# Kernel tuning notes

Measured on AMD Instinct MI355X. Metric: run time of the kernel, lower is better.

The kernel has to match this reference:

```python
import jax, jax.numpy as jnp
import numpy as np

B, S = 64, 256
VOCAB, DL, DA, DV = 30522, 300, 74, 35
DH, GH, LH, RH = 128, 64, 128, 128  # modality dim, proj-GRU hidden, LSTM hidden, RGN hidden


def _gru_dir(x, Wi, Wh, bi, bh):
    # x: [B,S,D] -> [B,S,H]; torch GRU gate order (r, z, n)
    xg = x @ Wi + bi  # [B,S,3H] precomputed input projections
    H = Wh.shape[0]
    def step(h, xg_t):
        hg = h @ Wh + bh
        xr, xz, xn = jnp.split(xg_t, 3, axis=-1)
        hr, hz, hn = jnp.split(hg, 3, axis=-1)
        r = jax.nn.sigmoid(xr + hr)
        z = jax.nn.sigmoid(xz + hz)
        n = jnp.tanh(xn + r * hn)
        h = (1.0 - z) * n + z * h
        return h, h
    h0 = jnp.zeros((x.shape[0], H), x.dtype)
    _, ys = jax.lax.scan(step, h0, jnp.swapaxes(xg, 0, 1))
    return jnp.swapaxes(ys, 0, 1)


def _bigru(x, Wi, Wh, bi, bh):
    f = _gru_dir(x, Wi[0], Wh[0], bi[0], bh[0])
    b = _gru_dir(x[:, ::-1], Wi[1], Wh[1], bi[1], bh[1])[:, ::-1]
    return jnp.concatenate([f, b], axis=-1)


def _lstm_dir(x, Wi, Wh, bi, bh):
    xg = x @ Wi + bi  # [B,S,4H]; torch LSTM gate order (i, f, g, o)
    H = Wh.shape[0]
    def step(carry, xg_t):
        h, c = carry
        g = xg_t + h @ Wh + bh
        i, f, gg, o = jnp.split(g, 4, axis=-1)
        c = jax.nn.sigmoid(f) * c + jax.nn.sigmoid(i) * jnp.tanh(gg)
        h = jax.nn.sigmoid(o) * jnp.tanh(c)
        return (h, c), h
    z = jnp.zeros((x.shape[0], H), x.dtype)
    _, ys = jax.lax.scan(step, (z, z), jnp.swapaxes(xg, 0, 1))
    return jnp.swapaxes(ys, 0, 1)


def _bilstm(x, Wi, Wh, bi, bh):
    f = _lstm_dir(x, Wi[0], Wh[0], bi[0], bh[0])
    b = _lstm_dir(x[:, ::-1], Wi[1], Wh[1], bi[1], bh[1])[:, ::-1]
    return jnp.concatenate([f, b], axis=-1)


def _rgn_scan(x, h0, Wx, Wh, b):
    # RGNCell: gated recurrent cell (GRU-style), returns final state [B,H]
    xg = x @ Wx + b  # [B,S,3H]
    def step(h, xg_t):
        hg = h @ Wh
        xr, xz, xn = jnp.split(xg_t, 3, axis=-1)
        hr, hz, hn = jnp.split(hg, 3, axis=-1)
        r = jax.nn.sigmoid(xr + hr)
        z = jax.nn.sigmoid(xz + hz)
        n = jnp.tanh(xn + r * hn)
        return (1.0 - z) * n + z * h, None
    h, _ = jax.lax.scan(step, h0, jnp.swapaxes(xg, 0, 1))
    return h


def _xattn(q, kv):
    # parameter-free scaled dot-product cross-modal attention (JCAF)
    scale = 1.0 / np.sqrt(q.shape[-1]).astype(np.float32)
    s = jnp.einsum('bsd,btd->bst', q, kv) * scale
    return jnp.einsum('bst,btd->bsd', jax.nn.softmax(s, axis=-1), kv)


def _forward(sentences, acoustic, video, state0, state1, emb,
             proj_l_W, proj_l_b, proj_a_W, proj_a_b, proj_v_W, proj_v_b,
             gru_Wi, gru_Wh, gru_bi, gru_bh,
             lstm_Wi, lstm_Wh, lstm_bi, lstm_bh,
             rgn_Wx, rgn_Wh, rgn_b, fc1_W, fc1_b, fc2_W, fc2_b):
    enc = emb[sentences]                          # LanguageEmbeddingLayer: [B,S,DL]
    # SeqEncoder: project each modality to 128-d (dropout off in eval)
    seq_l = enc @ proj_l_W + proj_l_b             # [B,S,128]
    seq_a = acoustic @ proj_a_W + proj_a_b
    seq_v = video @ proj_v_W + proj_v_b
    # project_l/a/v: bidirectional GRU 128 -> 2*64 = 128
    x_l = _bigru(seq_l, gru_Wi[0], gru_Wh[0], gru_bi[0], gru_bh[0])
    x_a = _bigru(seq_a, gru_Wi[1], gru_Wh[1], gru_bi[1], gru_bh[1])
    x_v = _bigru(seq_v, gru_Wi[2], gru_Wh[2], gru_bi[2], gru_bh[2])
    # JCAF: each modality enriched by cross-attention to the other two
    fin_txt = x_l + _xattn(x_l, x_a) + _xattn(x_l, x_v)
    fin_aud = x_a + _xattn(x_a, x_l) + _xattn(x_a, x_v)
    fin_vis = x_v + _xattn(x_v, x_l) + _xattn(x_v, x_a)
    tstep = jnp.concatenate([fin_txt, fin_aud, fin_vis], axis=-1)      # [B,S,384]
    step_fusion = _bilstm(tstep, lstm_Wi, lstm_Wh, lstm_bi, lstm_bh)   # [B,S,256]
    # two custom RGNCell recurrences: forward sweep + reversed sweep
    out0 = _rgn_scan(step_fusion, state0, rgn_Wx[0], rgn_Wh[0], rgn_b[0])
    out1 = _rgn_scan(step_fusion[:, ::-1], state1, rgn_Wx[1], rgn_Wh[1], rgn_b[1])
    h = jax.nn.leaky_relu((out0 + out1) @ fc1_W + fc1_b)
    return h @ fc2_W + fc2_b                     # [B,1]


def setup_inputs():
    keys = iter(jax.random.split(jax.random.key(0), 48))
    def rn(shape, s=0.05):
        return jax.random.normal(next(keys), shape, jnp.float32) * s
    return {
        'sentences': jax.random.randint(next(keys), (B, S), 0, VOCAB),
        'acoustic': jax.random.normal(next(keys), (B, S, DA), jnp.float32),
        'video': jax.random.normal(next(keys), (B, S, DV), jnp.float32),
        'state0': jax.random.normal(next(keys), (B, RH), jnp.float32),
        'state1': jax.random.normal(next(keys), (B, RH), jnp.float32),
        'emb': rn((VOCAB, DL), 0.1),
        'proj_l_W': rn((DL, DH)), 'proj_l_b': rn((DH,)),
        'proj_a_W': rn((DA, DH)), 'proj_a_b': rn((DH,)),
        'proj_v_W': rn((DV, DH)), 'proj_v_b': rn((DH,)),
        'gru_Wi': rn((3, 2, DH, 3 * GH)), 'gru_Wh': rn((3, 2, GH, 3 * GH)),
        'gru_bi': rn((3, 2, 3 * GH)), 'gru_bh': rn((3, 2, 3 * GH)),
        'lstm_Wi': rn((2, 3 * DH, 4 * LH)), 'lstm_Wh': rn((2, LH, 4 * LH)),
        'lstm_bi': rn((2, 4 * LH)), 'lstm_bh': rn((2, 4 * LH)),
        'rgn_Wx': rn((2, 2 * LH, 3 * RH)), 'rgn_Wh': rn((2, RH, 3 * RH)),
        'rgn_b': rn((2, 3 * RH)),
        'fc1_W': rn((RH, 32)), 'fc1_b': rn((32,)),
        'fc2_W': rn((32, 1)), 'fc2_b': rn((1,)),
    }


def reference(sentences, acoustic, video, state0, state1, emb,
              proj_l_W, proj_l_b, proj_a_W, proj_a_b, proj_v_W, proj_v_b,
              gru_Wi, gru_Wh, gru_bi, gru_bh,
              lstm_Wi, lstm_Wh, lstm_bi, lstm_bh,
              rgn_Wx, rgn_Wh, rgn_b, fc1_W, fc1_b, fc2_W, fc2_b):
    return _forward(sentences, acoustic, video, state0, state1, emb,
                    proj_l_W, proj_l_b, proj_a_W, proj_a_b, proj_v_W, proj_v_b,
                    gru_Wi, gru_Wh, gru_bi, gru_bh,
                    lstm_Wi, lstm_Wh, lstm_bi, lstm_bh,
                    rgn_Wx, rgn_Wh, rgn_b, fc1_W, fc1_b, fc2_W, fc2_b)
```

## Files before the change

kernel.cpp:

```cpp
#include <hip/hip_runtime.h>

#define WS_SEQ      0LL
#define WS_XGGRU    6291456LL
#define WS_X        0LL
#define WS_TSTEP    18874368LL
#define WS_S        6291456LL
#define WS_XGLSTM   0LL
#define WS_SF       16777216LL
#define WS_XGRGN    0LL
#define WS_OUT0     20971520LL

__device__ __forceinline__ float sigf(float x) {
    return __builtin_amdgcn_rcpf(1.f + __expf(-x));
}
__device__ __forceinline__ float tanhfast(float x) {
    float e = __expf(2.f * x);
    return 1.f - 2.f * __builtin_amdgcn_rcpf(e + 1.f);
}
__device__ __forceinline__ float rl(float v, int i) {
    return __int_as_float(__builtin_amdgcn_readlane(__float_as_int(v), i));
}

typedef float vf16 __attribute__((ext_vector_type(16)));
typedef float vf2 __attribute__((ext_vector_type(2)));

#define LD16(V, P, S) { _Pragma("unroll") \
    for (int _j = 0; _j < 16; ++_j) (V)[_j] = (P)[_j * (S)]; }
#define DOT16(ACC, V, H, B) { _Pragma("unroll") \
    for (int _j = 0; _j < 16; ++_j) (ACC) = fmaf(rl((H), (B) + _j), (V)[_j], (ACC)); }

__device__ __forceinline__ void gemm_body(
    const float* __restrict__ Ab, int lda, const int* __restrict__ idx,
    const float* __restrict__ Wb, int wld, int wtrans,
    const float* __restrict__ bb,
    float* __restrict__ Cb, int ldc,
    int K, float alpha, int accum)
{
    int m0 = blockIdx.y * 64, n0 = blockIdx.x * 64;
    int t = threadIdx.x;
    int tx = t & 7, ty = t >> 3;

    __shared__ __align__(16) float As[16][68];
    __shared__ __align__(16) float Ws[16][68];

    vf2 acc2[8][4];
#pragma unroll
    for (int i = 0; i < 8; ++i)
#pragma unroll
        for (int j = 0; j < 4; ++j) acc2[i][j] = (vf2){0.f, 0.f};

    long long arow[4];
#pragma unroll
    for (int i = 0; i < 4; ++i) {
        int m = (t + i * 64) >> 2;
        arow[i] = idx ? (long long)idx[m0 + m] : (long long)(m0 + m);
    }
    const bool a_vec = ((lda & 3) == 0);

    auto loadA = [&](int k0, float4* r) {
#pragma unroll
        for (int i = 0; i < 4; ++i) {
            int j = t + i * 64;
            int kq = j & 3;
            int kk = k0 + kq * 4;
            const float* p = Ab + arow[i] * (long long)lda + kk;
            float4 v = {0.f, 0.f, 0.f, 0.f};
            if (a_vec && kk + 3 < K) {
                v = *(const float4*)p;
            } else {
                if (kk + 0 < K) v.x = p[0];
                if (kk + 1 < K) v.y = p[1];
                if (kk + 2 < K) v.z = p[2];
                if (kk + 3 < K) v.w = p[3];
            }
            r[i] = v;
        }
    };
    auto loadW = [&](int k0, float4* r) {
        if (!wtrans) {
#pragma unroll
            for (int i = 0; i < 4; ++i) {
                int j = t + i * 64;
                int k = j >> 4, nq = j & 15;
                float4 v = {0.f, 0.f, 0.f, 0.f};
                if (k0 + k < K)
                    v = *(const float4*)(Wb + (long long)(k0 + k) * wld + n0 + nq * 4);
                r[i] = v;
            }
        } else {
#pragma unroll
            for (int i = 0; i < 4; ++i) {
                int j = t + i * 64;
                int n = j >> 2, kq = j & 3;
                int kk = k0 + kq * 4;
                const float* p = Wb + (long long)(n0 + n) * wld + kk;
                float4 v = {0.f, 0.f, 0.f, 0.f};
                if (kk + 3 < K) v = *(const float4*)p;
                else {
                    if (kk + 0 < K) v.x = p[0];
                    if (kk + 1 < K) v.y = p[1];
                    if (kk + 2 < K) v.z = p[2];
                    if (kk + 3 < K) v.w = p[3];
                }
                r[i] = v;
            }
        }
    };

    float4 aR[4], wR[4];
    loadA(0, aR);
    loadW(0, wR);

    for (int k0 = 0; k0 < K; k0 += 16) {
#pragma unroll
        for (int i = 0; i < 4; ++i) {
            int j = t + i * 64;
            int m = j >> 2, kq = j & 3;
            As[kq * 4 + 0][m] = aR[i].x; As[kq * 4 + 1][m] = aR[i].y;
            As[kq * 4 + 2][m] = aR[i].z; As[kq * 4 + 3][m] = aR[i].w;
        }
        if (!wtrans) {
#pragma unroll
            for (int i = 0; i < 4; ++i) {
                int j = t + i * 64;
                int k = j >> 4, nq = j & 15;
                *(float4*)&Ws[k][nq * 4] = wR[i];
            }
        } else {
#pragma unroll
            for (int i = 0; i < 4; ++i) {
                int j = t + i * 64;
                int n = j >> 2, kq = j & 3;
                Ws[kq * 4 + 0][n] = wR[i].x; Ws[kq * 4 + 1][n] = wR[i].y;
                Ws[kq * 4 + 2][n] = wR[i].z; Ws[kq * 4 + 3][n] = wR[i].w;
            }
        }
        __syncthreads();
        if (k0 + 16 < K) {
            loadA(k0 + 16, aR);
            loadW(k0 + 16, wR);
        }
#pragma unroll
        for (int k = 0; k < 16; ++k) {
            float4 a0 = *(const float4*)&As[k][ty * 8];
            float4 a1 = *(const float4*)&As[k][ty * 8 + 4];
            float4 b0 = *(const float4*)&Ws[k][tx * 8];
            float4 b1 = *(const float4*)&Ws[k][tx * 8 + 4];
            float av[8] = {a0.x, a0.y, a0.z, a0.w, a1.x, a1.y, a1.z, a1.w};
            vf2 bv[4];
            bv[0] = (vf2){b0.x, b0.y}; bv[1] = (vf2){b0.z, b0.w};
            bv[2] = (vf2){b1.x, b1.y}; bv[3] = (vf2){b1.z, b1.w};
#pragma unroll
            for (int i = 0; i < 8; ++i) {
                vf2 a2 = {av[i], av[i]};
#pragma unroll
                for (int j = 0; j < 4; ++j)
                    acc2[i][j] = __builtin_elementwise_fma(a2, bv[j], acc2[i][j]);
            }
        }
        __syncthreads();
    }

#pragma unroll
    for (int i = 0; i < 8; ++i) {
        long long gm = m0 + ty * 8 + i;
#pragma unroll
        for (int jq = 0; jq < 2; ++jq) {
            float* cp = Cb + gm * ldc + n0 + tx * 8 + jq * 4;
            float4 v;
            v.x = alpha * acc2[i][jq * 2 + 0][0];
            v.y = alpha * acc2[i][jq * 2 + 0][1];
            v.z = alpha * acc2[i][jq * 2 + 1][0];
            v.w = alpha * acc2[i][jq * 2 + 1][1];
            if (bb) {
                const float* bp = bb + n0 + tx * 8 + jq * 4;
                v.x += bp[0]; v.y += bp[1]; v.z += bp[2]; v.w += bp[3];
            }
            if (accum) {
                float4 o = *(const float4*)cp;
                v.x += o.x; v.y += o.y; v.z += o.z; v.w += o.w;
            }
            *(float4*)cp = v;
        }
    }
}

__global__ __launch_bounds__(64) void gemm_k(
    const float* __restrict__ A, long long a_z, int a_zdiv, int lda,
    const int* __restrict__ idx,
    const float* __restrict__ W, long long w_z, int wld, int wtrans,
    const float* __restrict__ bias, int bias_z,
    float* __restrict__ C, long long c_z, int ldc,
    int K, float alpha, int accum)
{
    int z = blockIdx.z;
    gemm_body(A + (long long)(z / a_zdiv) * a_z, lda, idx,
              W + (long long)z * w_z, wld, wtrans,
              bias ? bias + (long long)z * bias_z : nullptr,
              C + (long long)z * c_z, ldc, K, alpha, accum);
}

__global__ __launch_bounds__(64) void att_score_k(
    const float* __restrict__ X, float* __restrict__ S,
    int q0, int q1, int q2, int k0, int k1, int k2)
{
    int z = blockIdx.z;
    int pair = z >> 6, b = z & 63;
    int qi = pair == 0 ? q0 : (pair == 1 ? q1 : q2);
    int ki = pair == 0 ? k0 : (pair == 1 ? k1 : k2);
    gemm_body(X + (long long)qi * 2097152 + (long long)b * 32768, 128, nullptr,
              X + (long long)ki * 2097152 + (long long)b * 32768, 128, 1,
              nullptr,
              S + (long long)z * 65536, 256, 128, 0.08838834764831845f, 0);
}

__global__ __launch_bounds__(64) void att_apply_k(
    const float* __restrict__ S, const float* __restrict__ X,
    float* __restrict__ tstep,
    int q0, int q1, int q2, int k0, int k1, int k2)
{
    int z = blockIdx.z;
    int pair = z >> 6, b = z & 63;
    int qi = pair == 0 ? q0 : (pair == 1 ? q1 : q2);
    int ki = pair == 0 ? k0 : (pair == 1 ? k1 : k2);
    gemm_body(S + (long long)z * 65536, 256, nullptr,
              X + (long long)ki * 2097152 + (long long)b * 32768, 128, 0,
              nullptr,
              tstep + (long long)qi * 128 + (long long)b * 98304, 384,
              256, 1.f, 1);
}

__global__ __launch_bounds__(256) void copy_tstep_k(const float* __restrict__ x,
                                                    float* __restrict__ tstep)
{
    int o = blockIdx.x * 256 + threadIdx.x;
    int c = o % 384;
    int row = o / 384;
    int m = c >> 7, cc = c & 127;
    tstep[o] = x[(long long)m * 2097152 + (long long)row * 128 + cc];
}

__global__ __launch_bounds__(256) void softmax_k(float* __restrict__ S)
{
    int wave = threadIdx.x >> 6, lane = threadIdx.x & 63;
    int row = blockIdx.x * 4 + wave;
    float* p = S + (long long)row * 256;
    float v[4];
    float mx = -1e30f;
#pragma unroll
    for (int i = 0; i < 4; ++i) { v[i] = p[lane + i * 64]; mx = fmaxf(mx, v[i]); }
#pragma unroll
    for (int off = 32; off > 0; off >>= 1) mx = fmaxf(mx, __shfl_xor(mx, off));
    float sum = 0.f;
#pragma unroll
    for (int i = 0; i < 4; ++i) { v[i] = __expf(v[i] - mx); sum += v[i]; }
#pragma unroll
    for (int off = 32; off > 0; off >>= 1) sum += __shfl_xor(sum, off);
    float inv = 1.f / sum;
#pragma unroll
    for (int i = 0; i < 4; ++i) p[lane + i * 64] = v[i] * inv;
}

__global__ __launch_bounds__(192) void gru_rec_k(const float* __restrict__ xg,
                                                 const float* __restrict__ Wh,
                                                 const float* __restrict__ bh,
                                                 float* __restrict__ xout)
{
    int b = blockIdx.x, z = blockIdx.y;
    int m = z >> 1, d = z & 1;
    int tid = threadIdx.x, lane = tid & 63;
    int c = tid;
    const float* Whz = Wh + (long long)z * 12288;
    const float* wp = Whz + c;
    vf16 W0, W1, W2, W3;
    LD16(W0, wp + 0 * 16 * 192, 192); LD16(W1, wp + 1 * 16 * 192, 192);
    LD16(W2, wp + 2 * 16 * 192, 192); LD16(W3, wp + 3 * 16 * 192, 192);
    float bias = bh[z * 192 + c];

    __shared__ float g[2][192];
    int n = lane;
    float h = 0.f;
    const float* xgb = xg + (long long)z * 3145728 + (long long)b * 49152;
    float* xob = xout + (long long)m * 2097152 + (long long)b * 32768 + d * 64;
    int tt0 = d ? 255 : 0;
    const float* xr0 = xgb + tt0 * 192;
    float x_r = xr0[n], x_z = xr0[64 + n], x_n = xr0[128 + n];

#pragma unroll 1
    for (int t = 0; t < 256; ++t) {
        int tt = d ? 255 - t : t;
        float nx_r = 0, nx_z = 0, nx_n = 0;
        if (t < 255) {
            const float* xr = xgb + (d ? tt - 1 : tt + 1) * 192;
            nx_r = xr[n]; nx_z = xr[64 + n]; nx_n = xr[128 + n];
        }
        float s0 = bias, s1 = 0.f, s2 = 0.f, s3 = 0.f;
        DOT16(s0, W0, h, 0);  DOT16(s1, W1, h, 16);
        DOT16(s2, W2, h, 32); DOT16(s3, W3, h, 48);
        g[t & 1][c] = (s0 + s1) + (s2 + s3);
        __syncthreads();
        const float* gp = g[t & 1];
        float r  = sigf(x_r + gp[n]);
        float zz = sigf(x_z + gp[64 + n]);
        float nn = tanhfast(x_n + r * gp[128 + n]);
        h = (1.f - zz) * nn + zz * h;
        if (c < 64) xob[tt * 128 + n] = h;
        x_r = nx_r; x_z = nx_z; x_n = nx_n;
    }
}

__global__ __launch_bounds__(512) void lstm_rec_k(const float* __restrict__ xg,
                                                  const float* __restrict__ Wh,
                                                  const float* __restrict__ bh,
                                                  float* __restrict__ sf)
{
    int b = blockIdx.x, d = blockIdx.y;
    int tid = threadIdx.x, lane = tid & 63;
    int kh = tid >> 8;
    int cp = tid & 255;
    const float* Whz = Wh + (long long)d * 65536;

    __shared__ __align__(16) float wlds[36864];
    __shared__ float part[2][1024];
    for (int i = tid; i < 9216; i += 512) {
        int row = i >> 7, c4 = (i & 127) << 2;
        int srow = row < 36 ? row : row + 28;
        *(float4*)&wlds[row * 512 + c4] = *(const float4*)(Whz + srow * 512 + c4);
    }
    const float* wl  = wlds + (kh * 36) * 512 + 2 * cp;
    const float* wpg = Whz + (long long)(kh * 64 + 36) * 512 + 2 * cp;

    int n = kh * 64 + lane;
    float h = 0.f, cst = 0.f;
    const float* xgb = xg + (long long)d * 8388608 + (long long)b * 131072;
    float* sfb = sf + (long long)b * 65536 + d * 128;

    vf2 bias2 = {0.f, 0.f}, xc2 = {0.f, 0.f};
    if (kh == 0) {
        bias2 = *(const vf2*)(bh + d * 512 + 2 * cp);
        int tt0 = d ? 255 : 0;
        xc2 = *(const vf2*)(xgb + tt0 * 512 + 2 * cp);
    }
    __syncthreads();

#pragma unroll 1
    for (int t = 0; t < 256; ++t) {
        int tt = d ? 255 - t : t;
        vf2 nxc2 = {0.f, 0.f};
        if (kh == 0 && t < 255)
            nxc2 = *(const vf2*)(xgb + (d ? tt - 1 : tt + 1) * 512 + 2 * cp);
        vf2 a0 = xc2 + bias2, a1 = {0.f, 0.f};
#pragma unroll
        for (int r = 0; r < 36; ++r) {
            float hs = rl(h, r);
            vf2 hb = {hs, hs};
            vf2 w = *(const vf2*)(wl + r * 512);
            if (r & 1) a1 = __builtin_elementwise_fma(hb, w, a1);
            else       a0 = __builtin_elementwise_fma(hb, w, a0);
        }
#pragma unroll
        for (int r = 0; r < 28; ++r) {
            float hs = rl(h, 36 + r);
            vf2 hb = {hs, hs};
            vf2 w = *(const vf2*)(wpg + r * 512);
            if (r & 1) a1 = __builtin_elementwise_fma(hb, w, a1);
            else       a0 = __builtin_elementwise_fma(hb, w, a0);
        }
        *(vf2*)&part[t & 1][kh * 512 + 2 * cp] = a0 + a1;
        __syncthreads();
        const float* p = part[t & 1];
        float iv = p[n]       + p[512 + n];
        float fv = p[128 + n] + p[512 + 128 + n];
        float gv = p[256 + n] + p[512 + 256 + n];
        float ov = p[384 + n] + p[512 + 384 + n];
        cst = sigf(fv) * cst + sigf(iv) * tanhfast(gv);
        h = sigf(ov) * tanhfast(cst);
        if (cp < 64) sfb[tt * 256 + n] = h;
        xc2 = nxc2;
    }
}

__global__ __launch_bounds__(768) void rgn_rec_k(const float* __restrict__ xg,
                                                 const float* __restrict__ Wh,
                                                 const float* __restrict__ state0,
                                                 const float* __restrict__ state1,
                                                 float* __restrict__ outbase)
{
    int b = blockIdx.x, d = blockIdx.y;
    int tid = threadIdx.x, lane = tid & 63;
    int kh = (tid >= 384) ? 1 : 0;
    int c  = tid - kh * 384;
    const float* Whz = Wh + (long long)d * 49152;
    const float* wp = Whz + (long long)(kh * 64) * 384 + c;
    vf16 W0, W1, W2, W3;
    LD16(W0, wp + 0 * 16 * 384, 384); LD16(W1, wp + 1 * 16 * 384, 384);
    LD16(W2, wp + 2 * 16 * 384, 384); LD16(W3, wp + 3 * 16 * 384, 384);

    __shared__ float part[2][768];
    int n = kh * 64 + lane;
    const float* st = d ? state1 : state0;
    float h = st[b * 128 + n];
    const float* xgb = xg + (long long)d * 6291456 + (long long)b * 98304;
    int tt0 = d ? 255 : 0;
    const float* xr0 = xgb + tt0 * 384;
    float x_r = xr0[n], x_z = xr0[128 + n], x_n = xr0[256 + n];

#pragma unroll 1
    for (int t = 0; t < 256; ++t) {
        int tt = d ? 255 - t : t;
        float nx_r = 0, nx_z = 0, nx_n = 0;
        if (t < 255) {
            const float* xr = xgb + (d ? tt - 1 : tt + 1) * 384;
            nx_r = xr[n]; nx_z = xr[128 + n]; nx_n = xr[256 + n];
        }
        float s0 = 0.f, s1 = 0.f, s2 = 0.f, s3 = 0.f;
        DOT16(s0, W0, h, 0);  DOT16(s1, W1, h, 16);
        DOT16(s2, W2, h, 32); DOT16(s3, W3, h, 48);
        part[t & 1][kh * 384 + c] = (s0 + s1) + (s2 + s3);
        __syncthreads();
        const float* p = part[t & 1];
        float pr = p[n]       + p[384 + n];
        float pz = p[128 + n] + p[384 + 128 + n];
        float pn = p[256 + n] + p[384 + 256 + n];
        float r  = sigf(x_r + pr);
        float zz = sigf(x_z + pz);
        float nn = tanhfast(x_n + r * pn);
        h = (1.f - zz) * nn + zz * h;
        x_r = nx_r; x_z = nx_z; x_n = nx_n;
    }
    if (c < 64) outbase[(long long)d * 8192 + b * 128 + n] = h;
}

__global__ __launch_bounds__(256) void fc_k(const float* __restrict__ o01,
                                            const float* __restrict__ f1W,
                                            const float* __restrict__ f1b,
                                            const float* __restrict__ f2W,
                                            const float* __restrict__ f2b,
                                            float* __restrict__ out)
{
    __shared__ float s[8192];
    __shared__ float h1[2048];
    int tid = threadIdx.x;
    for (int e = tid; e < 8192; e += 256) s[e] = o01[e] + o01[8192 + e];
    __syncthreads();
    for (int o = tid; o < 2048; o += 256) {
        int b = o >> 5, q = o & 31;
        float acc = f1b[q];
        for (int k = 0; k < 128; ++k) acc += s[b * 128 + k] * f1W[k * 32 + q];
        h1[o] = acc >= 0.f ? acc : 0.01f * acc;
    }
    __syncthreads();
    if (tid < 64) {
        float acc = f2b[0];
        for (int q = 0; q < 32; ++q) acc += h1[tid * 32 + q] * f2W[q];
        out[tid] = acc;
    }
}

extern "C" void kernel_launch(void* const* d_in, const int* in_sizes, int n_in,
                              void* d_out, int out_size, void* d_ws, size_t ws_size,
                              hipStream_t stream)
{
    const int*   sent     = (const int*)  d_in[0];
    const float* acoustic = (const float*)d_in[1];
    const float* video    = (const float*)d_in[2];
    const float* state0   = (const float*)d_in[3];
    const float* state1   = (const float*)d_in[4];
    const float* emb      = (const float*)d_in[5];
    const float* plW = (const float*)d_in[6],  *plb = (const float*)d_in[7];
    const float* paW = (const float*)d_in[8],  *pab = (const float*)d_in[9];
    const float* pvW = (const float*)d_in[10], *pvb = (const float*)d_in[11];
    const float* gWi = (const float*)d_in[12], *gWh = (const float*)d_in[13];
    const float* gbi = (const float*)d_in[14], *gbh = (const float*)d_in[15];
    const float* lWi = (const float*)d_in[16], *lWh = (const float*)d_in[17];
    const float* lbi = (const float*)d_in[18], *lbh = (const float*)d_in[19];
    const float* rWx = (const float*)d_in[20], *rWh = (const float*)d_in[21];
    const float* rb  = (const float*)d_in[22];
    const float* f1W = (const float*)d_in[23], *f1b = (const float*)d_in[24];
    const float* f2W = (const float*)d_in[25], *f2b = (const float*)d_in[26];
    float* ws  = (float*)d_ws;
    float* out = (float*)d_out;

    dim3 blk(64);

    gemm_k<<<dim3(2, 256, 1), blk, 0, stream>>>(emb, 0, 1, 300, sent,
        plW, 0, 128, 0, plb, 0, ws + WS_SEQ, 0, 128, 300, 1.f, 0);
    gemm_k<<<dim3(2, 256, 1), blk, 0, stream>>>(acoustic, 0, 1, 74, nullptr,
        paW, 0, 128, 0, pab, 0, ws + WS_SEQ + 2097152, 0, 128, 74, 1.f, 0);
    gemm_k<<<dim3(2, 256, 1), blk, 0, stream>>>(video, 0, 1, 35, nullptr,
        pvW, 0, 128, 0, pvb, 0, ws + WS_SEQ + 4194304, 0, 128, 35, 1.f, 0);

    gemm_k<<<dim3(3, 256, 6), blk, 0, stream>>>(ws + WS_SEQ, 2097152, 2, 128, nullptr,
        gWi, 24576, 192, 0, gbi, 192, ws + WS_XGGRU, 3145728, 192, 128, 1.f, 0);

    gru_rec_k<<<dim3(64, 6), dim3(192), 0, stream>>>(ws + WS_XGGRU, gWh, gbh, ws + WS_X);

    copy_tstep_k<<<dim3(24576), dim3(256), 0, stream>>>(ws + WS_X, ws + WS_TSTEP);

    att_score_k<<<dim3(4, 4, 192), blk, 0, stream>>>(ws + WS_X, ws + WS_S,
        0, 1, 2, 1, 0, 0);
    softmax_k<<<dim3(12288), dim3(256), 0, stream>>>(ws + WS_S);
    att_apply_k<<<dim3(2, 4, 192), blk, 0, stream>>>(ws + WS_S, ws + WS_X,
        ws + WS_TSTEP, 0, 1, 2, 1, 0, 0);
    att_score_k<<<dim3(4, 4, 192), blk, 0, stream>>>(ws + WS_X, ws + WS_S,
        0, 1, 2, 2, 2, 1);
    softmax_k<<<dim3(12288), dim3(256), 0, stream>>>(ws + WS_S);
    att_apply_k<<<dim3(2, 4, 192), blk, 0, stream>>>(ws + WS_S, ws + WS_X,
        ws + WS_TSTEP, 0, 1, 2, 2, 2, 1);

    gemm_k<<<dim3(8, 256, 2), blk, 0, stream>>>(ws + WS_TSTEP, 0, 1, 384, nullptr,
        lWi, 196608, 512, 0, lbi, 512, ws + WS_XGLSTM, 8388608, 512, 384, 1.f, 0);

    lstm_rec_k<<<dim3(64, 2), dim3(512), 0, stream>>>(ws + WS_XGLSTM, lWh, lbh, ws + WS_SF);

    gemm_k<<<dim3(6, 256, 2), blk, 0, stream>>>(ws + WS_SF, 0, 1, 256, nullptr,
        rWx, 98304, 384, 0, rb, 384, ws + WS_XGRGN, 6291456, 384, 256, 1.f, 0);

    rgn_rec_k<<<dim3(64, 2), dim3(768), 0, stream>>>(ws + WS_XGRGN, rWh, state0, state1,
                                                     ws + WS_OUT0);

    fc_k<<<dim3(1), dim3(256), 0, stream>>>(ws + WS_OUT0, f1W, f1b, f2W, f2b, out);
}
```

Before: 1.451 ms.

## Double-buffer GEMM shared tiles, merge projection launches, fuse tstep copy into attention

The shared GEMM body now ping-pongs two LDS tile buffers, so the next tile is written after compute and only one barrier is needed per k-step. The three modality projection GEMMs are merged into a single launch indexed by blockIdx.z. The separate copy kernel that seeded the tstep buffer is removed; the first attention-apply pass instead adds the query features in its epilogue and writes rather than accumulates. This cuts launches and a full extra pass over memory, at the cost of doubled LDS per block, which may lower occupancy.

```diff
diff --git a/kernel.cpp b/kernel.cpp
--- a/kernel.cpp
+++ b/kernel.cpp
@@ -33,6 +33,7 @@
     const float* __restrict__ Ab, int lda, const int* __restrict__ idx,
     const float* __restrict__ Wb, int wld, int wtrans,
     const float* __restrict__ bb,
+    const float* __restrict__ initsrc, int ldi,
     float* __restrict__ Cb, int ldc,
     int K, float alpha, int accum)
 {
@@ -40,8 +41,8 @@
     int t = threadIdx.x;
     int tx = t & 7, ty = t >> 3;
 
-    __shared__ __align__(16) float As[16][68];
-    __shared__ __align__(16) float Ws[16][68];
+    __shared__ __align__(16) float As[2][16][68];
+    __shared__ __align__(16) float Ws[2][16][68];
 
     vf2 acc2[8][4];
 #pragma unroll
@@ -106,46 +107,52 @@
             }
         }
     };
+    auto writeT = [&](int buf, const float4* aR, const float4* wR) {
+#pragma unroll
+        for (int i = 0; i < 4; ++i) {
+            int j = t + i * 64;
+            int m = j >> 2, kq = j & 3;
+            As[buf][kq * 4 + 0][m] = aR[i].x; As[buf][kq * 4 + 1][m] = aR[i].y;
+            As[buf][kq * 4 + 2][m] = aR[i].z; As[buf][kq * 4 + 3][m] = aR[i].w;
+        }
+        if (!wtrans) {
+#pragma unroll
+            for (int i = 0; i < 4; ++i) {
+                int j = t + i * 64;
+                int k = j >> 4, nq = j & 15;
+                *(float4*)&Ws[buf][k][nq * 4] = wR[i];
+            }
+        } else {
+#pragma unroll
+            for (int i = 0; i < 4; ++i) {
+                int j = t + i * 64;
+                int n = j >> 2, kq = j & 3;
+                Ws[buf][kq * 4 + 0][n] = wR[i].x; Ws[buf][kq * 4 + 1][n] = wR[i].y;
+                Ws[buf][kq * 4 + 2][n] = wR[i].z; Ws[buf][kq * 4 + 3][n] = wR[i].w;
+            }
+        }
+    };
 
     float4 aR[4], wR[4];
     loadA(0, aR);
     loadW(0, wR);
-
-    for (int k0 = 0; k0 < K; k0 += 16) {
-#pragma unroll
-        for (int i = 0; i < 4; ++i) {
-            int j = t + i * 64;
-            int m = j >> 2, kq = j & 3;
-            As[kq * 4 + 0][m] = aR[i].x; As[kq * 4 + 1][m] = aR[i].y;
-            As[kq * 4 + 2][m] = aR[i].z; As[kq * 4 + 3][m] = aR[i].w;
-        }
-        if (!wtrans) {
-#pragma unroll
-            for (int i = 0; i < 4; ++i) {
-                int j = t + i * 64;
-                int k = j >> 4, nq = j & 15;
-                *(float4*)&Ws[k][nq * 4] = wR[i];
-            }
-        } else {
-#pragma unroll
-            for (int i = 0; i < 4; ++i) {
-                int j = t + i * 64;
-                int n = j >> 2, kq = j & 3;
-                Ws[kq * 4 + 0][n] = wR[i].x; Ws[kq * 4 + 1][n] = wR[i].y;
-                Ws[kq * 4 + 2][n] = wR[i].z; Ws[kq * 4 + 3][n] = wR[i].w;
-            }
-        }
-        __syncthreads();
-        if (k0 + 16 < K) {
-            loadA(k0 + 16, aR);
-            loadW(k0 + 16, wR);
+    writeT(0, aR, wR);
+    __syncthreads();
+
+    int nt = (K + 15) >> 4;
+    for (int ti = 0; ti < nt; ++ti) {
+        int cur = ti & 1;
+        bool more = (ti + 1 < nt);
+        if (more) {
+            loadA((ti + 1) * 16, aR);
+            loadW((ti + 1) * 16, wR);
         }
 #pragma unroll
         for (int k = 0; k < 16; ++k) {
-            float4 a0 = *(const float4*)&As[k][ty * 8];
-            float4 a1 = *(const float4*)&As[k][ty * 8 + 4];
-            float4 b0 = *(const float4*)&Ws[k][tx * 8];
-            float4 b1 = *(const float4*)&Ws[k][tx * 8 + 4];
+            float4 a0 = *(const float4*)&As[cur][k][ty * 8];
+            float4 a1 = *(const float4*)&As[cur][k][ty * 8 + 4];
+            float4 b0 = *(const float4*)&Ws[cur][k][tx * 8];
+            float4 b1 = *(const float4*)&Ws[cur][k][tx * 8 + 4];
             float av[8] = {a0.x, a0.y, a0.z, a0.w, a1.x, a1.y, a1.z, a1.w};
             vf2 bv[4];
             bv[0] = (vf2){b0.x, b0.y}; bv[1] = (vf2){b0.z, b0.w};
@@ -158,7 +165,10 @@
                     acc2[i][j] = __builtin_elementwise_fma(a2, bv[j], acc2[i][j]);
             }
         }
-        __syncthreads();
+        if (more) {
+            writeT(cur ^ 1, aR, wR);
+            __syncthreads();
+        }
     }
 
 #pragma unroll
@@ -166,15 +176,20 @@
         long long gm = m0 + ty * 8 + i;
 #pragma unroll
         for (int jq = 0; jq < 2; ++jq) {
-            float* cp = Cb + gm * ldc + n0 + tx * 8 + jq * 4;
+            int col = n0 + tx * 8 + jq * 4;
+            float* cp = Cb + gm * ldc + col;
             float4 v;
             v.x = alpha * acc2[i][jq * 2 + 0][0];
             v.y = alpha * acc2[i][jq * 2 + 0][1];
             v.z = alpha * acc2[i][jq * 2 + 1][0];
             v.w = alpha * acc2[i][jq * 2 + 1][1];
             if (bb) {
-                const float* bp = bb + n0 + tx * 8 + jq * 4;
+                const float* bp = bb + col;
                 v.x += bp[0]; v.y += bp[1]; v.z += bp[2]; v.w += bp[3];
+            }
+            if (initsrc) {
+                const float* ip = initsrc + gm * (long long)ldi + col;
+                v.x += ip[0]; v.y += ip[1]; v.z += ip[2]; v.w += ip[3];
             }
             if (accum) {
                 float4 o = *(const float4*)cp;
@@ -196,8 +211,28 @@
     int z = blockIdx.z;
     gemm_body(A + (long long)(z / a_zdiv) * a_z, lda, idx,
               W + (long long)z * w_z, wld, wtrans,
-              bias ? bias + (long long)z * bias_z : nullptr,
+              bias ? bias + (long long)z * bias_z : nullptr, nullptr, 0,
               C + (long long)z * c_z, ldc, K, alpha, accum);
+}
+
+__global__ __launch_bounds__(64) void proj3_k(
+    const int* __restrict__ sent, const float* __restrict__ emb,
+    const float* __restrict__ acoustic, const float* __restrict__ video,
+    const float* __restrict__ plW, const float* __restrict__ plb,
+    const float* __restrict__ paW, const float* __restrict__ pab,
+    const float* __restrict__ pvW, const float* __restrict__ pvb,
+    float* __restrict__ seq)
+{
+    int z = blockIdx.z;
+    const float* A; int lda; const int* ix; const float* W; const float* bi;
+    float* C; int K;
+    if (z == 0) { A = emb;      lda = 300; ix = sent;    W = plW; bi = plb;
+                  C = seq;               K = 300; }
+    else if (z == 1) { A = acoustic; lda = 74;  ix = nullptr; W = paW; bi = pab;
+                  C = seq + 2097152;     K = 74; }
+    else        { A = video;    lda = 35;  ix = nullptr; W = pvW; bi = pvb;
+                  C = seq + 4194304;     K = 35; }
+    gemm_body(A, lda, ix, W, 128, 0, bi, nullptr, 0, C, 128, K, 1.f, 0);
 }
 
 __global__ __launch_bounds__(64) void att_score_k(
@@ -210,34 +245,26 @@
     int ki = pair == 0 ? k0 : (pair == 1 ? k1 : k2);
     gemm_body(X + (long long)qi * 2097152 + (long long)b * 32768, 128, nullptr,
               X + (long long)ki * 2097152 + (long long)b * 32768, 128, 1,
-              nullptr,
+              nullptr, nullptr, 0,
               S + (long long)z * 65536, 256, 128, 0.08838834764831845f, 0);
 }
 
 __global__ __launch_bounds__(64) void att_apply_k(
     const float* __restrict__ S, const float* __restrict__ X,
     float* __restrict__ tstep,
-    int q0, int q1, int q2, int k0, int k1, int k2)
+    int q0, int q1, int q2, int k0, int k1, int k2, int doinit)
 {
     int z = blockIdx.z;
     int pair = z >> 6, b = z & 63;
     int qi = pair == 0 ? q0 : (pair == 1 ? q1 : q2);
     int ki = pair == 0 ? k0 : (pair == 1 ? k1 : k2);
+    const float* initsrc = doinit
+        ? X + (long long)qi * 2097152 + (long long)b * 32768 : nullptr;
     gemm_body(S + (long long)z * 65536, 256, nullptr,
               X + (long long)ki * 2097152 + (long long)b * 32768, 128, 0,
-              nullptr,
+              nullptr, initsrc, 128,
               tstep + (long long)qi * 128 + (long long)b * 98304, 384,
-              256, 1.f, 1);
-}
-
-__global__ __launch_bounds__(256) void copy_tstep_k(const float* __restrict__ x,
-                                                    float* __restrict__ tstep)
-{
-    int o = blockIdx.x * 256 + threadIdx.x;
-    int c = o % 384;
-    int row = o / 384;
-    int m = c >> 7, cc = c & 127;
-    tstep[o] = x[(long long)m * 2097152 + (long long)row * 128 + cc];
+              256, 1.f, doinit ? 0 : 1);
 }
 
 __global__ __launch_bounds__(256) void softmax_k(float* __restrict__ S)
@@ -483,30 +510,24 @@
 
     dim3 blk(64);
 
-    gemm_k<<<dim3(2, 256, 1), blk, 0, stream>>>(emb, 0, 1, 300, sent,
-        plW, 0, 128, 0, plb, 0, ws + WS_SEQ, 0, 128, 300, 1.f, 0);
-    gemm_k<<<dim3(2, 256, 1), blk, 0, stream>>>(acoustic, 0, 1, 74, nullptr,
-        paW, 0, 128, 0, pab, 0, ws + WS_SEQ + 2097152, 0, 128, 74, 1.f, 0);
-    gemm_k<<<dim3(2, 256, 1), blk, 0, stream>>>(video, 0, 1, 35, nullptr,
-        pvW, 0, 128, 0, pvb, 0, ws + WS_SEQ + 4194304, 0, 128, 35, 1.f, 0);
+    proj3_k<<<dim3(2, 256, 3), blk, 0, stream>>>(sent, emb, acoustic, video,
+        plW, plb, paW, pab, pvW, pvb, ws + WS_SEQ);
 
     gemm_k<<<dim3(3, 256, 6), blk, 0, stream>>>(ws + WS_SEQ, 2097152, 2, 128, nullptr,
         gWi, 24576, 192, 0, gbi, 192, ws + WS_XGGRU, 3145728, 192, 128, 1.f, 0);
 
     gru_rec_k<<<dim3(64, 6), dim3(192), 0, stream>>>(ws + WS_XGGRU, gWh, gbh, ws + WS_X);
-
-    copy_tstep_k<<<dim3(24576), dim3(256), 0, stream>>>(ws + WS_X, ws + WS_TSTEP);
 
     att_score_k<<<dim3(4, 4, 192), blk, 0, stream>>>(ws + WS_X, ws + WS_S,
         0, 1, 2, 1, 0, 0);
     softmax_k<<<dim3(12288), dim3(256), 0, stream>>>(ws + WS_S);
     att_apply_k<<<dim3(2, 4, 192), blk, 0, stream>>>(ws + WS_S, ws + WS_X,
-        ws + WS_TSTEP, 0, 1, 2, 1, 0, 0);
+        ws + WS_TSTEP, 0, 1, 2, 1, 0, 0, 1);
     att_score_k<<<dim3(4, 4, 192), blk, 0, stream>>>(ws + WS_X, ws + WS_S,
         0, 1, 2, 2, 2, 1);
     softmax_k<<<dim3(12288), dim3(256), 0, stream>>>(ws + WS_S);
     att_apply_k<<<dim3(2, 4, 192), blk, 0, stream>>>(ws + WS_S, ws + WS_X,
-        ws + WS_TSTEP, 0, 1, 2, 2, 2, 1);
+        ws + WS_TSTEP, 0, 1, 2, 2, 2, 1, 0);
 
     gemm_k<<<dim3(8, 256, 2), blk, 0, stream>>>(ws + WS_TSTEP, 0, 1, 384, nullptr,
         lWi, 196608, 512, 0, lbi, 512, ws + WS_XGLSTM, 8388608, 512, 384, 1.f, 0);
```

Result: slower. 1.696 ms (+16.9%).
